# Kernel tuning notes

Hardware: AMD Instinct MI355X
Metric: run time of the kernel (lower is better)

Reference implementation:

```python
import jax, jax.numpy as jnp
import numpy as np
import math, itertools

RANGE = 1.0
DIM = 3
N_LEVELS = 16
N_FEATS = 2
HASHMAP_SIZE = 2 ** 15
BASE_RES = 16
FINEST_RES = 512
_b = math.exp((math.log(FINEST_RES) - math.log(BASE_RES)) / (N_LEVELS - 1))
RESOLUTIONS = [int(math.floor(BASE_RES * (_b ** i))) for i in range(N_LEVELS)]
PRIMES = np.array([1, 2654435761, 805459861], dtype=np.uint32)
# True -> take the lower corner (xi) along that dim, weight (1 - xf)
BIN_MASK = np.array(list(itertools.product([1, 0], repeat=DIM)), dtype=bool)  # (8, 3)


def setup_inputs() -> dict:
    key = jax.random.key(0)
    kx, kt = jax.random.split(key)
    x = jax.random.uniform(kx, (1048576, DIM), jnp.float32, minval=-RANGE, maxval=RANGE)
    # per-level hash tables (nn.Embedding weights), stacked: (L, 2^15, F)
    tables = jax.random.normal(kt, (N_LEVELS, HASHMAP_SIZE, N_FEATS), jnp.float32) * 0.01
    return {"x": x, "tables": tables}


def _encode_level(x01, table, res):
    # x01: (N, 3) in [0, 1];  table: (2^15, F)
    xs = x01 * res
    xi_f = jnp.floor(xs)
    xf = (xs - xi_f)[:, None, :]                       # (N, 1, 3) fractional part
    xi = xi_f.astype(jnp.uint32)[:, None, :]           # (N, 1, 3)
    mask = jnp.asarray(BIN_MASK)[None]                 # (1, 8, 3)
    corners = jnp.where(mask, xi, xi + jnp.uint32(1))  # (N, 8, 3)
    ws = jnp.prod(jnp.where(mask, 1.0 - xf, xf), axis=-1)  # (N, 8) trilinear weights
    h = corners * jnp.asarray(PRIMES)                  # uint32 mul with wraparound
    idx = (h[..., 0] ^ h[..., 1] ^ h[..., 2]) % jnp.uint32(HASHMAP_SIZE)  # (N, 8)
    feats = table[idx]                                 # (N, 8, F) irregular gather
    return jnp.sum(feats * ws[..., None], axis=-2)     # (N, F)


def reference(x, tables):
    # HashGridLoRAEncoder.forward: normalize to [0,1], encode, concat levels
    x01 = (x + RANGE) / (2.0 * RANGE)                  # (N, 3)
    outs = [_encode_level(x01, tables[i], RESOLUTIONS[i]) for i in range(N_LEVELS)]
    return jnp.concatenate(outs, axis=-1)              # (N, 32)
```

## Files before the change

kernel.cpp:

```cpp
#include <hip/hip_runtime.h>

#define TMASK 32767u
#define P2 2654435761u
#define P3 805459861u

typedef float f32x4 __attribute__((ext_vector_type(4)));
typedef unsigned u32x4 __attribute__((ext_vector_type(4)));

constexpr int NBINS = 32768;
constexpr int BLOCK = 128;
constexpr int HP = 17;

constexpr size_t WS_HIST   = 0;
constexpr size_t WS_CURSOR = 128 * 1024;
constexpr size_t WS_KEYR   = 256 * 1024;
constexpr size_t WS_PERM   = WS_KEYR + (size_t)1048576 * 4;
constexpr size_t WS_NEEDED = WS_PERM + (size_t)1048576 * 4;

__device__ __forceinline__ unsigned part1by2(unsigned v) {
    v &= 0x3FFu;
    v = (v | (v << 16)) & 0x030000FFu;
    v = (v | (v << 8))  & 0x0300F00Fu;
    v = (v | (v << 4))  & 0x030C30C3u;
    v = (v | (v << 2))  & 0x09249249u;
    return v;
}

__device__ __forceinline__ unsigned morton_key(float px, float py, float pz) {
    const float x01 = (px + 1.0f) * 0.5f;
    const float y01 = (py + 1.0f) * 0.5f;
    const float z01 = (pz + 1.0f) * 0.5f;
    const unsigned cx = min(31u, (unsigned)(x01 * 32.0f));
    const unsigned cy = min(31u, (unsigned)(y01 * 32.0f));
    const unsigned cz = min(31u, (unsigned)(z01 * 32.0f));
    return part1by2(cx) | (part1by2(cy) << 1) | (part1by2(cz) << 2);
}

__global__ __launch_bounds__(256) void hist_kernel(const float* __restrict__ xin,
                                                   unsigned* __restrict__ hist,
                                                   unsigned* __restrict__ keyrank, int n) {
    const int j = blockIdx.x * blockDim.x + threadIdx.x;
    const int p0 = j * 4;
    if (p0 + 3 < n) {
        const f32x4* xb = (const f32x4*)(xin + (size_t)p0 * 3);
        const f32x4 a = xb[0];
        const f32x4 b = xb[1];
        const f32x4 c = xb[2];
        const unsigned k0 = morton_key(a[0], a[1], a[2]);
        const unsigned k1 = morton_key(a[3], b[0], b[1]);
        const unsigned k2 = morton_key(b[2], b[3], c[0]);
        const unsigned k3 = morton_key(c[1], c[2], c[3]);
        const unsigned r0 = atomicAdd(&hist[k0], 1u);
        const unsigned r1 = atomicAdd(&hist[k1], 1u);
        const unsigned r2 = atomicAdd(&hist[k2], 1u);
        const unsigned r3 = atomicAdd(&hist[k3], 1u);
        u32x4 kr = { (r0 << 15) | k0, (r1 << 15) | k1,
                     (r2 << 15) | k2, (r3 << 15) | k3 };
        *(u32x4*)(keyrank + p0) = kr;
    } else {
        for (int p = p0; p < n; ++p) {
            const size_t bb = 3ull * (size_t)p;
            const unsigned k = morton_key(xin[bb], xin[bb + 1], xin[bb + 2]);
            const unsigned r = atomicAdd(&hist[k], 1u);
            keyrank[p] = (r << 15) | k;
        }
    }
}

__global__ __launch_bounds__(1024) void scan_kernel(const unsigned* __restrict__ hist,
                                                    unsigned* __restrict__ cursor) {
    const int t = threadIdx.x;
    const u32x4* h4 = (const u32x4*)hist;
    u32x4 v[8];
    #pragma unroll
    for (int k = 0; k < 8; ++k) v[k] = h4[t * 8 + k];

    unsigned loc[32];
    unsigned s = 0;
    #pragma unroll
    for (int k = 0; k < 8; ++k) {
        loc[4 * k + 0] = s; s += v[k][0];
        loc[4 * k + 1] = s; s += v[k][1];
        loc[4 * k + 2] = s; s += v[k][2];
        loc[4 * k + 3] = s; s += v[k][3];
    }

    const int lane = t & 63;
    unsigned inc = s;
    #pragma unroll
    for (int off = 1; off < 64; off <<= 1) {
        const unsigned u = __shfl_up(inc, off, 64);
        if (lane >= off) inc += u;
    }

    __shared__ unsigned wtot[16];
    if (lane == 63) wtot[t >> 6] = inc;
    __syncthreads();
    if (t < 16) {
        unsigned w = wtot[t];
        const unsigned orig = w;
        #pragma unroll
        for (int off = 1; off < 16; off <<= 1) {
            const unsigned u = __shfl_up(w, off, 16);
            if (t >= off) w += u;
        }
        wtot[t] = w - orig;
    }
    __syncthreads();

    const unsigned base = wtot[t >> 6] + (inc - s);
    u32x4* c4 = (u32x4*)cursor;
    #pragma unroll
    for (int k = 0; k < 8; ++k) {
        u32x4 o = { base + loc[4 * k + 0], base + loc[4 * k + 1],
                    base + loc[4 * k + 2], base + loc[4 * k + 3] };
        c4[t * 8 + k] = o;
    }
}

__global__ __launch_bounds__(256) void scatter_kernel(const unsigned* __restrict__ keyrank,
                                                      const unsigned* __restrict__ cursor,
                                                      unsigned* __restrict__ perm, int n) {
    const int j = blockIdx.x * blockDim.x + threadIdx.x;
    const int p0 = j * 4;
    if (p0 + 3 < n) {
        const u32x4 kr = *(const u32x4*)(keyrank + p0);
        #pragma unroll
        for (int q = 0; q < 4; ++q) {
            const unsigned key  = kr[q] & TMASK;
            const unsigned rank = kr[q] >> 15;
            perm[cursor[key] + rank] = (unsigned)(p0 + q);
        }
    } else {
        for (int p = p0; p < n; ++p) {
            const unsigned krv  = keyrank[p];
            perm[cursor[krv & TMASK] + (krv >> 15)] = (unsigned)p;
        }
    }
}

__global__ __launch_bounds__(BLOCK, 8) void hashgrid_kernel(
    const float* __restrict__ xin, const unsigned* __restrict__ perm,
    const float* __restrict__ tables, float* __restrict__ out, int n, int sorted)
{
    __shared__ float lds[BLOCK * HP];
    __shared__ unsigned sorig[BLOCK];
    const int t = threadIdx.x;
    const int base = blockIdx.x * BLOCK;
    const int i = base + t;

    float px = 0.f, py = 0.f, pz = 0.f;
    unsigned orig = (unsigned)i;
    if (i < n) {
        if (sorted) orig = perm[i];
        const size_t xb = 3ull * (size_t)orig;
        if ((int)orig + 1 < n) {
            const f32x4 v = *(const f32x4*)(xin + xb);
            px = v[0]; py = v[1]; pz = v[2];
        } else {
            px = xin[xb]; py = xin[xb + 1]; pz = xin[xb + 2];
        }
    }
    sorig[t] = orig;

    const float x01 = (px + 1.0f) * 0.5f;
    const float y01 = (py + 1.0f) * 0.5f;
    const float z01 = (pz + 1.0f) * 0.5f;

    constexpr int RES[16] = {16, 20, 25, 32, 40, 50, 64, 80,
                             101, 128, 161, 203, 256, 322, 406, 512};

    const int nf4 = min(n - base, BLOCK) * 4;

    #pragma unroll
    for (int h = 0; h < 2; ++h) {
        #pragma unroll
        for (int lo = 0; lo < 8; ++lo) {
            const int l = h * 8 + lo;
            const float rf = (float)RES[l];
            const float xs = x01 * rf, ys = y01 * rf, zs = z01 * rf;
            const float fxs = floorf(xs), fys = floorf(ys), fzs = floorf(zs);
            const float tx = xs - fxs, ty = ys - fys, tz = zs - fzs;
            const unsigned xi = (unsigned)fxs;
            const unsigned yi = (unsigned)fys;
            const unsigned zi = (unsigned)fzs;

            const unsigned hx0 = xi & TMASK;
            const unsigned hym = yi * P2;
            const unsigned hy0 = hym & TMASK;
            const unsigned hy1 = (hym + P2) & TMASK;
            const unsigned hzm = zi * P3;
            const unsigned hz0 = hzm & TMASK;
            const unsigned hz1 = (hzm + P3) & TMASK;

            const float wx0 = 1.f - tx, wy0 = 1.f - ty, wz0 = 1.f - tz;
            const bool xeven = (xi & 1u) == 0u;
            const float* tbl = tables + (size_t)l * 65536ull;

            float a0 = 0.f, a1 = 0.f;
            #pragma unroll
            for (int p = 0; p < 4; ++p) {
                const unsigned m  = ((p & 1) ? hy1 : hy0) ^ ((p & 2) ? hz1 : hz0);
                const float  wyz  = ((p & 1) ? ty : wy0) * ((p & 2) ? tz : wz0);
                const unsigned idx0 = hx0 ^ m;
                const unsigned e    = idx0 & ~1u;
                const f32x4 q = *(const f32x4*)(tbl + 2u * e);
                const bool lo2 = (idx0 & 1u) == 0u;
                const float c0x = lo2 ? q[0] : q[2];
                const float c0y = lo2 ? q[1] : q[3];
                float c1x, c1y;
                if (xeven) {
                    c1x = lo2 ? q[2] : q[0];
                    c1y = lo2 ? q[3] : q[1];
                } else {
                    const unsigned idx1 = (hx0 + 1u) ^ m;
                    const float2 f = *(const float2*)(tbl + 2u * idx1);
                    c1x = f.x; c1y = f.y;
                }
                const float w0 = wyz * wx0;
                const float w1 = wyz * tx;
                a0 = fmaf(w0, c0x, fmaf(w1, c1x, a0));
                a1 = fmaf(w0, c0y, fmaf(w1, c1y, a1));
            }
            lds[t * HP + 2 * lo]     = a0;
            lds[t * HP + 2 * lo + 1] = a1;
        }

        __syncthreads();

        #pragma unroll
        for (int j = 0; j < 4; ++j) {
            const int g = j * BLOCK + t;
            if (g < nf4) {
                const int p = g >> 2;
                const int e = (g & 3) * 4;
                const float* s = &lds[p * HP + e];
                f32x4 v = { s[0], s[1], s[2], s[3] };
                __builtin_nontemporal_store(
                    v, (f32x4*)(out + (size_t)sorig[p] * 32ull + (size_t)(h * 16 + e)));
            }
        }
        __syncthreads();
    }
}

extern "C" void kernel_launch(void* const* d_in, const int* in_sizes, int n_in,
                              void* d_out, int out_size, void* d_ws, size_t ws_size,
                              hipStream_t stream) {
    const float* x      = (const float*)d_in[0];
    const float* tables = (const float*)d_in[1];
    float* out          = (float*)d_out;

    const int n = in_sizes[0] / 3;
    const int sorted = (ws_size >= WS_NEEDED) ? 1 : 0;

    unsigned* perm = (unsigned*)((char*)d_ws + WS_PERM);

    if (sorted) {
        unsigned* hist    = (unsigned*)((char*)d_ws + WS_HIST);
        unsigned* cursor  = (unsigned*)((char*)d_ws + WS_CURSOR);
        unsigned* keyrank = (unsigned*)((char*)d_ws + WS_KEYR);
        const int nq = (n + 3) / 4;
        hipMemsetAsync(hist, 0, NBINS * sizeof(unsigned), stream);
        hipLaunchKernelGGL(hist_kernel, dim3((nq + 255) / 256), dim3(256), 0, stream,
                           x, hist, keyrank, n);
        hipLaunchKernelGGL(scan_kernel, dim3(1), dim3(1024), 0, stream, hist, cursor);
        hipLaunchKernelGGL(scatter_kernel, dim3((nq + 255) / 256), dim3(256), 0, stream,
                           keyrank, cursor, perm, n);
    }

    hipLaunchKernelGGL(hashgrid_kernel, dim3((n + BLOCK - 1) / BLOCK), dim3(BLOCK), 0, stream,
                       x, perm, tables, out, n, sorted);
}
```

Baseline: 353.1 us.

## Refine Morton sort to 64^3 cells and scatter coordinates with index payload

Raises the Morton sort grid from 32^3 to 64^3 cells, so points in the same block are more spatially coherent and hash table gathers get better cache locality. The scatter step now writes each point's coordinates plus its original index as a float4 into a sorted buffer, so the main kernel reads contiguously instead of doing an indirect gather through a permutation. In exchange the histogram and scan grow eightfold and run in a single 1024-thread block with a serial 256-entry loop per thread, and the workspace requirement grows. A permutation-only fallback is kept for smaller workspaces.

```diff
diff --git a/kernel.cpp b/kernel.cpp
--- a/kernel.cpp
+++ b/kernel.cpp
@@ -1,5 +1,6 @@
 #include <hip/hip_runtime.h>
 
+#define KMASK 0x3FFFFu
 #define TMASK 32767u
 #define P2 2654435761u
 #define P3 805459861u
@@ -7,15 +8,16 @@
 typedef float f32x4 __attribute__((ext_vector_type(4)));
 typedef unsigned u32x4 __attribute__((ext_vector_type(4)));
 
-constexpr int NBINS = 32768;
+constexpr int NBINS = 262144;
 constexpr int BLOCK = 128;
 constexpr int HP = 17;
 
 constexpr size_t WS_HIST   = 0;
-constexpr size_t WS_CURSOR = 128 * 1024;
-constexpr size_t WS_KEYR   = 256 * 1024;
-constexpr size_t WS_PERM   = WS_KEYR + (size_t)1048576 * 4;
-constexpr size_t WS_NEEDED = WS_PERM + (size_t)1048576 * 4;
+constexpr size_t WS_CURSOR = (size_t)1 << 20;
+constexpr size_t WS_KEYR   = (size_t)2 << 20;
+constexpr size_t WS_DATA   = (size_t)6 << 20;
+constexpr size_t WS_NEED_PAYLOAD = WS_DATA + (size_t)1048576 * 16;
+constexpr size_t WS_NEED_PERM    = WS_DATA + (size_t)1048576 * 4;
 
 __device__ __forceinline__ unsigned part1by2(unsigned v) {
     v &= 0x3FFu;
@@ -30,9 +32,9 @@
     const float x01 = (px + 1.0f) * 0.5f;
     const float y01 = (py + 1.0f) * 0.5f;
     const float z01 = (pz + 1.0f) * 0.5f;
-    const unsigned cx = min(31u, (unsigned)(x01 * 32.0f));
-    const unsigned cy = min(31u, (unsigned)(y01 * 32.0f));
-    const unsigned cz = min(31u, (unsigned)(z01 * 32.0f));
+    const unsigned cx = min(63u, (unsigned)(x01 * 64.0f));
+    const unsigned cy = min(63u, (unsigned)(y01 * 64.0f));
+    const unsigned cz = min(63u, (unsigned)(z01 * 64.0f));
     return part1by2(cx) | (part1by2(cy) << 1) | (part1by2(cz) << 2);
 }
 
@@ -54,15 +56,15 @@
         const unsigned r1 = atomicAdd(&hist[k1], 1u);
         const unsigned r2 = atomicAdd(&hist[k2], 1u);
         const unsigned r3 = atomicAdd(&hist[k3], 1u);
-        u32x4 kr = { (r0 << 15) | k0, (r1 << 15) | k1,
-                     (r2 << 15) | k2, (r3 << 15) | k3 };
+        u32x4 kr = { (r0 << 18) | k0, (r1 << 18) | k1,
+                     (r2 << 18) | k2, (r3 << 18) | k3 };
         *(u32x4*)(keyrank + p0) = kr;
     } else {
         for (int p = p0; p < n; ++p) {
             const size_t bb = 3ull * (size_t)p;
             const unsigned k = morton_key(xin[bb], xin[bb + 1], xin[bb + 2]);
             const unsigned r = atomicAdd(&hist[k], 1u);
-            keyrank[p] = (r << 15) | k;
+            keyrank[p] = (r << 18) | k;
         }
     }
 }
@@ -71,18 +73,12 @@
                                                     unsigned* __restrict__ cursor) {
     const int t = threadIdx.x;
     const u32x4* h4 = (const u32x4*)hist;
-    u32x4 v[8];
-    #pragma unroll
-    for (int k = 0; k < 8; ++k) v[k] = h4[t * 8 + k];
-
-    unsigned loc[32];
+
     unsigned s = 0;
-    #pragma unroll
-    for (int k = 0; k < 8; ++k) {
-        loc[4 * k + 0] = s; s += v[k][0];
-        loc[4 * k + 1] = s; s += v[k][1];
-        loc[4 * k + 2] = s; s += v[k][2];
-        loc[4 * k + 3] = s; s += v[k][3];
+    #pragma unroll 8
+    for (int k = 0; k < 64; ++k) {
+        const u32x4 v = h4[t * 64 + k];
+        s += v[0] + v[1] + v[2] + v[3];
     }
 
     const int lane = t & 63;
@@ -108,40 +104,72 @@
     }
     __syncthreads();
 
-    const unsigned base = wtot[t >> 6] + (inc - s);
+    unsigned run = wtot[t >> 6] + (inc - s);
     u32x4* c4 = (u32x4*)cursor;
-    #pragma unroll
-    for (int k = 0; k < 8; ++k) {
-        u32x4 o = { base + loc[4 * k + 0], base + loc[4 * k + 1],
-                    base + loc[4 * k + 2], base + loc[4 * k + 3] };
-        c4[t * 8 + k] = o;
-    }
-}
-
-__global__ __launch_bounds__(256) void scatter_kernel(const unsigned* __restrict__ keyrank,
-                                                      const unsigned* __restrict__ cursor,
-                                                      unsigned* __restrict__ perm, int n) {
+    #pragma unroll 8
+    for (int k = 0; k < 64; ++k) {
+        const u32x4 v = h4[t * 64 + k];
+        u32x4 o;
+        o[0] = run;           run += v[0];
+        o[1] = run;           run += v[1];
+        o[2] = run;           run += v[2];
+        o[3] = run;           run += v[3];
+        c4[t * 64 + k] = o;
+    }
+}
+
+__global__ __launch_bounds__(256) void scatter_payload_kernel(
+    const float* __restrict__ xin, const unsigned* __restrict__ keyrank,
+    const unsigned* __restrict__ cursor, f32x4* __restrict__ sortedx, int n) {
+    const int j = blockIdx.x * blockDim.x + threadIdx.x;
+    const int p0 = j * 4;
+    if (p0 + 3 < n) {
+        const f32x4* xb = (const f32x4*)(xin + (size_t)p0 * 3);
+        const f32x4 a = xb[0];
+        const f32x4 b = xb[1];
+        const f32x4 c = xb[2];
+        const u32x4 kr = *(const u32x4*)(keyrank + p0);
+        const float X[4] = { a[0], a[3], b[2], c[1] };
+        const float Y[4] = { a[1], b[0], b[3], c[2] };
+        const float Z[4] = { a[2], b[1], c[0], c[3] };
+        #pragma unroll
+        for (int q = 0; q < 4; ++q) {
+            const unsigned slot = cursor[kr[q] & KMASK] + (kr[q] >> 18);
+            f32x4 v = { X[q], Y[q], Z[q], __uint_as_float((unsigned)(p0 + q)) };
+            sortedx[slot] = v;
+        }
+    } else {
+        for (int p = p0; p < n; ++p) {
+            const size_t bb = 3ull * (size_t)p;
+            const unsigned krv = keyrank[p];
+            const unsigned slot = cursor[krv & KMASK] + (krv >> 18);
+            f32x4 v = { xin[bb], xin[bb + 1], xin[bb + 2], __uint_as_float((unsigned)p) };
+            sortedx[slot] = v;
+        }
+    }
+}
+
+__global__ __launch_bounds__(256) void scatter_perm_kernel(
+    const unsigned* __restrict__ keyrank, const unsigned* __restrict__ cursor,
+    unsigned* __restrict__ perm, int n) {
     const int j = blockIdx.x * blockDim.x + threadIdx.x;
     const int p0 = j * 4;
     if (p0 + 3 < n) {
         const u32x4 kr = *(const u32x4*)(keyrank + p0);
         #pragma unroll
-        for (int q = 0; q < 4; ++q) {
-            const unsigned key  = kr[q] & TMASK;
-            const unsigned rank = kr[q] >> 15;
-            perm[cursor[key] + rank] = (unsigned)(p0 + q);
-        }
+        for (int q = 0; q < 4; ++q)
+            perm[cursor[kr[q] & KMASK] + (kr[q] >> 18)] = (unsigned)(p0 + q);
     } else {
         for (int p = p0; p < n; ++p) {
-            const unsigned krv  = keyrank[p];
-            perm[cursor[krv & TMASK] + (krv >> 15)] = (unsigned)p;
+            const unsigned krv = keyrank[p];
+            perm[cursor[krv & KMASK] + (krv >> 18)] = (unsigned)p;
         }
     }
 }
 
 __global__ __launch_bounds__(BLOCK, 8) void hashgrid_kernel(
-    const float* __restrict__ xin, const unsigned* __restrict__ perm,
-    const float* __restrict__ tables, float* __restrict__ out, int n, int sorted)
+    const float* __restrict__ xin, const void* __restrict__ sdata,
+    const float* __restrict__ tables, float* __restrict__ out, int n, int mode)
 {
     __shared__ float lds[BLOCK * HP];
     __shared__ unsigned sorig[BLOCK];
@@ -152,13 +180,19 @@
     float px = 0.f, py = 0.f, pz = 0.f;
     unsigned orig = (unsigned)i;
     if (i < n) {
-        if (sorted) orig = perm[i];
-        const size_t xb = 3ull * (size_t)orig;
-        if ((int)orig + 1 < n) {
-            const f32x4 v = *(const f32x4*)(xin + xb);
+        if (mode == 2) {
+            const f32x4 v = ((const f32x4*)sdata)[i];
             px = v[0]; py = v[1]; pz = v[2];
+            orig = __float_as_uint(v[3]);
         } else {
-            px = xin[xb]; py = xin[xb + 1]; pz = xin[xb + 2];
+            if (mode == 1) orig = ((const unsigned*)sdata)[i];
+            const size_t xb = 3ull * (size_t)orig;
+            if ((int)orig + 1 < n) {
+                const f32x4 v = *(const f32x4*)(xin + xb);
+                px = v[0]; py = v[1]; pz = v[2];
+            } else {
+                px = xin[xb]; py = xin[xb + 1]; pz = xin[xb + 2];
+            }
         }
     }
     sorig[t] = orig;
@@ -252,11 +286,14 @@
     float* out          = (float*)d_out;
 
     const int n = in_sizes[0] / 3;
-    const int sorted = (ws_size >= WS_NEEDED) ? 1 : 0;
-
-    unsigned* perm = (unsigned*)((char*)d_ws + WS_PERM);
-
-    if (sorted) {
+
+    int mode = 0;
+    if (ws_size >= WS_NEED_PAYLOAD)    mode = 2;
+    else if (ws_size >= WS_NEED_PERM)  mode = 1;
+
+    void* sdata = (char*)d_ws + WS_DATA;
+
+    if (mode) {
         unsigned* hist    = (unsigned*)((char*)d_ws + WS_HIST);
         unsigned* cursor  = (unsigned*)((char*)d_ws + WS_CURSOR);
         unsigned* keyrank = (unsigned*)((char*)d_ws + WS_KEYR);
@@ -265,10 +302,14 @@
         hipLaunchKernelGGL(hist_kernel, dim3((nq + 255) / 256), dim3(256), 0, stream,
                            x, hist, keyrank, n);
         hipLaunchKernelGGL(scan_kernel, dim3(1), dim3(1024), 0, stream, hist, cursor);
-        hipLaunchKernelGGL(scatter_kernel, dim3((nq + 255) / 256), dim3(256), 0, stream,
-                           keyrank, cursor, perm, n);
+        if (mode == 2)
+            hipLaunchKernelGGL(scatter_payload_kernel, dim3((nq + 255) / 256), dim3(256),
+                               0, stream, x, keyrank, cursor, (f32x4*)sdata, n);
+        else
+            hipLaunchKernelGGL(scatter_perm_kernel, dim3((nq + 255) / 256), dim3(256),
+                               0, stream, keyrank, cursor, (unsigned*)sdata, n);
     }
 
     hipLaunchKernelGGL(hashgrid_kernel, dim3((n + BLOCK - 1) / BLOCK), dim3(BLOCK), 0, stream,
-                       x, perm, tables, out, n, sorted);
-}
+                       x, sdata, tables, out, n, mode);
+}
```

New measurement: 429.2 us. +21.6%, slower.
